# Kernel optimization log

Hardware: AMD Instinct MI355X
Metric: run time of the kernel (lower is better)

The kernel has to match this reference:

```python
import jax, jax.numpy as jnp
import numpy as np

B, S, H, NH, G = 2, 2048, 2048, 16, 2
HD = H // NH          # head_dim = 128
NKV = NH // G         # kv heads = 8
EPS = 1e-6


def setup_inputs() -> dict:
    key = jax.random.key(0)
    ks = jax.random.split(key, 5)
    sc = 0.02
    return {
        "x": jax.random.normal(ks[0], (B, S, H), jnp.float32),
        "wq": jax.random.normal(ks[1], (H, H), jnp.float32) * sc,
        "wk": jax.random.normal(ks[2], (H, H // G), jnp.float32) * sc,
        "wv": jax.random.normal(ks[3], (H, H // G), jnp.float32) * sc,
        "wo": jax.random.normal(ks[4], (H, H), jnp.float32) * sc,
        "rms_w": jnp.ones((HD,), jnp.float32),
        "token_positions": jnp.arange(S, dtype=jnp.int32),
    }


def _rmsnorm(x, w):
    # x: (b, s, HD, n_heads); normalize over the head_dim axis (axis 2)
    ms = jnp.mean(x * x, axis=2, keepdims=True)
    return x * jax.lax.rsqrt(ms + EPS) * w[None, None, :, None]


def _rope(x, pos):
    # x: (b, s, HD, n); interleaved-pair rotation along HD, base 10000
    half = HD // 2
    inv_freq = 1.0 / (10000.0 ** (jnp.arange(half, dtype=jnp.float32) * 2.0 / HD))
    ang = pos.astype(jnp.float32)[:, None] * inv_freq[None, :]   # (s, HD/2)
    cos = jnp.cos(ang)[None, :, :, None]
    sin = jnp.sin(ang)[None, :, :, None]
    x1 = x[:, :, 0::2, :]
    x2 = x[:, :, 1::2, :]
    r1 = x1 * cos - x2 * sin
    r2 = x1 * sin + x2 * cos
    return jnp.stack([r1, r2], axis=3).reshape(x.shape)


def reference(x, wq, wk, wv, wo, rms_w, token_positions):
    b, s, _ = x.shape
    # projections, split hidden as (head_dim, n_heads) exactly like the torch .view
    q = (x @ wq).reshape(b, s, HD, NH)
    k = (x @ wk).reshape(b, s, HD, NKV)
    v = (x @ wv).reshape(b, s, HD, NKV)
    # per-head RMSNorm (over head_dim) then RoPE on Q and K
    q = _rope(_rmsnorm(q, rms_w), token_positions)
    k = _rope(_rmsnorm(k, rms_w), token_positions)
    # grouped-query attention: group G query heads per kv head
    q5 = q.reshape(b, s, HD, NKV, G)
    scores = jnp.einsum('bsdkg,btdk->bkgst', q5, k)          # (b,NKV,G,s,s)
    mask = jnp.triu(jnp.ones((s, s), bool), 1)               # causal
    scores = jnp.where(mask[None, None, None], -jnp.inf, scores)
    attn = jax.nn.softmax(scores / jnp.sqrt(jnp.float32(HD)), axis=-1)
    ctx = jnp.einsum('bkgst,btdk->bkgsd', attn, v)           # (b,NKV,G,s,HD)
    ctx = ctx.reshape(b, NH, s, HD).transpose(0, 2, 1, 3).reshape(b, s, H)
    return ctx @ wo
```

## Files before the change

kernel.cpp:

```cpp
#include <hip/hip_runtime.h>
#include <hip/hip_bf16.h>
#include <stdint.h>

typedef unsigned short u16;
typedef uint32_t u32;
typedef __attribute__((ext_vector_type(8))) short s8v;
typedef __attribute__((ext_vector_type(4))) float f4v;
typedef __attribute__((ext_vector_type(4))) unsigned int u4v;

#define SQ   2048
#define HDIM 2048
#define HD_  128
#define NH_  16
#define NKV_ 8

__device__ __forceinline__ u16 f2b(float f) {
  uint32_t u = __builtin_bit_cast(uint32_t, f);
  u += 0x7fffu + ((u >> 16) & 1u);
  return (u16)(u >> 16);
}
__device__ __forceinline__ float b2f(u16 v) {
  uint32_t u = ((uint32_t)v) << 16;
  return __builtin_bit_cast(float, u);
}
__device__ __forceinline__ u32 pk2(float lo, float hi) {
  return (u32)f2b(lo) | ((u32)f2b(hi) << 16);
}
__device__ __forceinline__ u32 cvtpk(float lo, float hi) {
  u32 r;
  asm("v_cvt_pk_bf16_f32 %0, %1, %2" : "=v"(r) : "v"(lo), "v"(hi));
  return r;
}

__global__ __launch_bounds__(256) void k_cast(const float* __restrict__ in,
                                              u16* __restrict__ out, int n4) {
  int i = blockIdx.x * 256 + threadIdx.x;
  if (i >= n4) return;
  f4v v = *(const f4v*)(in + (size_t)i * 4);
  union { u16 s[4]; uint64_t u; } o;
  o.s[0] = f2b(v[0]); o.s[1] = f2b(v[1]); o.s[2] = f2b(v[2]); o.s[3] = f2b(v[3]);
  *(uint64_t*)(out + (size_t)i * 4) = o.u;
}

__global__ __launch_bounds__(256) void k_transpose4(const float* __restrict__ wq,
                                                    const float* __restrict__ wk,
                                                    const float* __restrict__ wv,
                                                    const float* __restrict__ wo,
                                                    u16* __restrict__ wqt,
                                                    u16* __restrict__ wkt,
                                                    u16* __restrict__ wvt,
                                                    u16* __restrict__ wot) {
  const int z = blockIdx.z;
  const float* in = (z == 0) ? wq : (z == 1) ? wk : (z == 2) ? wv : wo;
  u16* out = (z == 0) ? wqt : (z == 1) ? wkt : (z == 2) ? wvt : wot;
  const int cols = (z == 1 || z == 2) ? 1024 : 2048;
  int c0 = blockIdx.x * 32, r0 = blockIdx.y * 32;
  if (c0 >= cols) return;
  __shared__ float tile[32][33];
  int tx = threadIdx.x & 31, ty = threadIdx.x >> 5;
#pragma unroll
  for (int i = 0; i < 32; i += 8)
    tile[ty + i][tx] = in[(size_t)(r0 + ty + i) * cols + c0 + tx];
  __syncthreads();
#pragma unroll
  for (int i = 0; i < 32; i += 8)
    out[(size_t)(c0 + ty + i) * 2048 + r0 + tx] = f2b(tile[tx][ty + i]);
}

template <int F32OUT>
__global__ __launch_bounds__(256) void k_gemm(const u16* __restrict__ A,
                                              const u16* __restrict__ Bt,
                                              void* __restrict__ C,
                                              int M, int N, int K) {
  __shared__ __align__(16) u16 As[128 * 64];
  __shared__ __align__(16) u16 Bs[128 * 64];
  const int tid = threadIdx.x;
  const int lane = tid & 63, wvi = tid >> 6;
  const int wm = wvi >> 1, wn = wvi & 1;
  const int l15 = lane & 15, l4 = lane >> 4;
  const int m0 = blockIdx.y * 128, n0 = blockIdx.x * 128;
  auto* As3 = (__attribute__((address_space(3))) char*)As;
  auto* Bs3 = (__attribute__((address_space(3))) char*)Bs;
  int srow[4], soff[4];
#pragma unroll
  for (int i = 0; i < 4; i++) {
    int slot = wvi * 4096 + i * 1024 + lane * 16;
    int r = slot >> 7;
    int gc = ((slot >> 4) & 7) ^ (r & 7);
    srow[i] = r; soff[i] = gc * 16;
  }
  f4v acc[4][4] = {};
  for (int k0 = 0; k0 < K; k0 += 64) {
#pragma unroll
    for (int i = 0; i < 4; i++) {
      const char* gA = (const char*)(A + (size_t)(m0 + srow[i]) * K + k0) + soff[i];
      const char* gB = (const char*)(Bt + (size_t)(n0 + srow[i]) * K + k0) + soff[i];
      __builtin_amdgcn_global_load_lds((__attribute__((address_space(1))) void*)gA,
                                       (__attribute__((address_space(3))) void*)(As3 + wvi * 4096 + i * 1024),
                                       16, 0, 0);
      __builtin_amdgcn_global_load_lds((__attribute__((address_space(1))) void*)gB,
                                       (__attribute__((address_space(3))) void*)(Bs3 + wvi * 4096 + i * 1024),
                                       16, 0, 0);
    }
    __syncthreads();
#pragma unroll
    for (int kk = 0; kk < 2; kk++) {
      s8v af[4], bf[4];
#pragma unroll
      for (int i = 0; i < 4; i++) {
        int ra = wm * 64 + i * 16 + l15;
        af[i] = *(const s8v*)((const char*)As + ra * 128 +
                              ((kk * 64 + l4 * 16) ^ ((ra & 7) << 4)));
        int rb = wn * 64 + i * 16 + l15;
        bf[i] = *(const s8v*)((const char*)Bs + rb * 128 +
                              ((kk * 64 + l4 * 16) ^ ((rb & 7) << 4)));
      }
#pragma unroll
      for (int i = 0; i < 4; i++)
#pragma unroll
        for (int j = 0; j < 4; j++)
          acc[i][j] = __builtin_amdgcn_mfma_f32_16x16x32_bf16(af[i], bf[j], acc[i][j], 0, 0, 0);
    }
    __syncthreads();
  }
#pragma unroll
  for (int i = 0; i < 4; i++) {
#pragma unroll
    for (int j = 0; j < 4; j++) {
      int mb = m0 + wm * 64 + i * 16 + l4 * 4;
      int nn = n0 + wn * 64 + j * 16 + l15;
#pragma unroll
      for (int r = 0; r < 4; r++) {
        float v = acc[i][j][r];
        if (F32OUT) ((float*)C)[(size_t)(mb + r) * N + nn] = v;
        else        ((u16*)C)[(size_t)(mb + r) * N + nn]  = f2b(v);
      }
    }
  }
}

__global__ __launch_bounds__(512, 2) void k_gemm256(const u16* __restrict__ A,
                                                    const u16* __restrict__ Bt,
                                                    u16* __restrict__ C,
                                                    int M, int N, int K) {
  __shared__ __align__(16) u16 Al[2][256 * 64];
  __shared__ __align__(16) u16 Bl[2][256 * 64];
  const int tid = threadIdx.x;
  const int lane = tid & 63, wid = tid >> 6;
  const int wm = wid >> 2, wn = wid & 3;
  const int l15 = lane & 15, l4 = lane >> 4;
  const int m0 = blockIdx.y * 256, n0 = blockIdx.x * 256;
  auto* A3 = (__attribute__((address_space(3))) char*)&Al[0][0];
  auto* B3 = (__attribute__((address_space(3))) char*)&Bl[0][0];
  int srow[4], soff[4];
#pragma unroll
  for (int j = 0; j < 4; j++) {
    int slot = j * 8192 + tid * 16;
    srow[j] = slot >> 7;
    soff[j] = (((slot >> 4) & 7) ^ (srow[j] & 7)) * 16;
  }
  int xk2[2];
#pragma unroll
  for (int ks = 0; ks < 2; ks++) xk2[ks] = (((ks * 4 + l4) ^ (l15 & 7)) << 4);

#define STAGE256(buf, k0s)                                                        \
  do {                                                                            \
    _Pragma("unroll")                                                             \
    for (int j = 0; j < 4; j++) {                                                 \
      const char* gA = (const char*)(A + (size_t)(m0 + srow[j]) * K + (k0s)) + soff[j]; \
      __builtin_amdgcn_global_load_lds(                                           \
          (const __attribute__((address_space(1))) void*)gA,                      \
          (__attribute__((address_space(3))) void*)(A3 + (buf) * 32768 + j * 8192 + tid * 16), \
          16, 0, 0);                                                              \
      const char* gB = (const char*)(Bt + (size_t)(n0 + srow[j]) * K + (k0s)) + soff[j]; \
      __builtin_amdgcn_global_load_lds(                                           \
          (const __attribute__((address_space(1))) void*)gB,                      \
          (__attribute__((address_space(3))) void*)(B3 + (buf) * 32768 + j * 8192 + tid * 16), \
          16, 0, 0);                                                              \
    }                                                                             \
  } while (0)

  f4v acc[8][4] = {};
  STAGE256(0, 0);
  STAGE256(1, 64);
  const int nK = K >> 6;
  for (int t = 0; t < nK; t++) {
    if (t == nK - 1) asm volatile("s_waitcnt vmcnt(0)" ::: "memory");
    else             asm volatile("s_waitcnt vmcnt(8)" ::: "memory");
    __builtin_amdgcn_s_barrier();
    __builtin_amdgcn_sched_barrier(0);
    const char* Ab = (const char*)&Al[0][0] + (t & 1) * 32768;
    const char* Bb = (const char*)&Bl[0][0] + (t & 1) * 32768;
#pragma unroll
    for (int qm = 0; qm < 2; qm++)
#pragma unroll
      for (int qn = 0; qn < 2; qn++) {
        s8v af[4][2], bf2[2][2];
#pragma unroll
        for (int i2 = 0; i2 < 4; i2++) {
          int row = wm * 128 + (qm * 4 + i2) * 16 + l15;
#pragma unroll
          for (int ks = 0; ks < 2; ks++)
            af[i2][ks] = *(const s8v*)(Ab + row * 128 + xk2[ks]);
        }
#pragma unroll
        for (int j2 = 0; j2 < 2; j2++) {
          int row = wn * 64 + (qn * 2 + j2) * 16 + l15;
#pragma unroll
          for (int ks = 0; ks < 2; ks++)
            bf2[j2][ks] = *(const s8v*)(Bb + row * 128 + xk2[ks]);
        }
        __builtin_amdgcn_s_setprio(1);
#pragma unroll
        for (int i2 = 0; i2 < 4; i2++)
#pragma unroll
          for (int j2 = 0; j2 < 2; j2++)
#pragma unroll
            for (int ks = 0; ks < 2; ks++)
              acc[qm * 4 + i2][qn * 2 + j2] = __builtin_amdgcn_mfma_f32_16x16x32_bf16(
                  af[i2][ks], bf2[j2][ks], acc[qm * 4 + i2][qn * 2 + j2], 0, 0, 0);
        __builtin_amdgcn_s_setprio(0);
      }
    __builtin_amdgcn_sched_barrier(0);
    if (t + 2 < nK) {
      __builtin_amdgcn_s_barrier();
      STAGE256(t & 1, (t + 2) * 64);
    }
  }
#undef STAGE256
#pragma unroll
  for (int mi = 0; mi < 8; mi++)
#pragma unroll
    for (int ni = 0; ni < 4; ni++) {
      int mb = m0 + wm * 128 + mi * 16 + l4 * 4;
      int nn = n0 + wn * 64 + ni * 16 + l15;
#pragma unroll
      for (int r = 0; r < 4; r++)
        C[(size_t)(mb + r) * N + nn] = f2b(acc[mi][ni][r]);
    }
}

__global__ __launch_bounds__(256) void k_normrope(const u16* __restrict__ qkv,
                                                  const float* __restrict__ rms_w,
                                                  const int* __restrict__ pos_arr,
                                                  u16* __restrict__ qq,
                                                  u16* __restrict__ kko,
                                                  u16* __restrict__ vto) {
  int idx = blockIdx.x;
  int b = idx >> 11, s = idx & 2047;
  int t = threadIdx.x;
  __shared__ float part[256];
  __shared__ float rstdq[16], rstdk[8];
  __shared__ float lcos[64], lsin[64];
  float pos = (float)pos_arr[s];
  if (t < 64) {
    float ang = pos * exp2f(-0.20762050593046f * (float)t);
    float sn, cs;
    sincosf(ang, &sn, &cs);
    lcos[t] = cs; lsin[t] = sn;
  }
  const u16* qr = qkv + (size_t)idx * 4096;
  const u16* kr = qr + 2048;
  const u16* vr = qr + 3072;
  int h = t & 15, ch = t >> 4;
  float qv[8]; float ss = 0.f;
#pragma unroll
  for (int j = 0; j < 8; j++) {
    float v = b2f(qr[(ch * 8 + j) * 16 + h]);
    qv[j] = v; ss += v * v;
  }
  part[t] = ss;
  __syncthreads();
  if (t < 16) {
    float tot = 0.f;
#pragma unroll
    for (int c = 0; c < 16; c++) tot += part[c * 16 + t];
    rstdq[t] = rsqrtf(tot * (1.f / 128.f) + 1e-6f);
  }
  __syncthreads();
  {
    float rs = rstdq[h];
    s8v ov;
#pragma unroll
    for (int p = 0; p < 4; p++) {
      int d0 = ch * 8 + p * 2;
      float v0 = qv[p * 2]     * rs * rms_w[d0];
      float v1 = qv[p * 2 + 1] * rs * rms_w[d0 + 1];
      float cs = lcos[d0 >> 1], sn = lsin[d0 >> 1];
      ov[p * 2]     = (short)f2b((v0 * cs - v1 * sn) * 0.08838834764831845f);
      ov[p * 2 + 1] = (short)f2b((v0 * sn + v1 * cs) * 0.08838834764831845f);
    }
    *(s8v*)(qq + ((size_t)(b * 16 + h) * SQ + s) * HD_ + ch * 8) = ov;
  }
  __syncthreads();
  int kv = t & 7, ch2 = t >> 3;
  float kvs[8]; float ssk = 0.f;
  if (t < 128) {
#pragma unroll
    for (int j = 0; j < 8; j++) {
      float v = b2f(kr[(ch2 * 8 + j) * 8 + kv]);
      kvs[j] = v; ssk += v * v;
    }
    part[t] = ssk;
  }
  __syncthreads();
  if (t < 8) {
    float tot = 0.f;
#pragma unroll
    for (int c = 0; c < 16; c++) tot += part[c * 8 + t];
    rstdk[t] = rsqrtf(tot * (1.f / 128.f) + 1e-6f);
  }
  __syncthreads();
  if (t < 128) {
    float rs = rstdk[kv];
    s8v ov;
#pragma unroll
    for (int p = 0; p < 4; p++) {
      int d0 = ch2 * 8 + p * 2;
      float v0 = kvs[p * 2]     * rs * rms_w[d0];
      float v1 = kvs[p * 2 + 1] * rs * rms_w[d0 + 1];
      float cs = lcos[d0 >> 1], sn = lsin[d0 >> 1];
      ov[p * 2]     = (short)f2b(v0 * cs - v1 * sn);
      ov[p * 2 + 1] = (short)f2b(v0 * sn + v1 * cs);
    }
    *(s8v*)(kko + ((size_t)(b * 8 + kv) * SQ + s) * HD_ + ch2 * 8) = ov;
#pragma unroll
    for (int j = 0; j < 8; j++) {
      int d = ch2 * 8 + j;
      vto[((size_t)(b * 8 + kv) * HD_ + d) * SQ + s] = vr[d * 8 + kv];
    }
  }
}

__global__ __launch_bounds__(512, 2) void k_attn(const u16* __restrict__ qq,
                                                 const u16* __restrict__ kk,
                                                 const u16* __restrict__ vt,
                                                 u16* __restrict__ ctx) {
  const int tile = (blockIdx.z == 1) ? (15 - (int)blockIdx.x) : (int)blockIdx.x;
  const int s0 = tile * 128;
  const int h  = blockIdx.y;
  const int b  = blockIdx.z;
  const int kvh = h >> 1;
  const int tid = threadIdx.x, lane = tid & 63, w = tid >> 6;
  const int l15 = lane & 15, l4 = lane >> 4;
  __shared__ __align__(16) u16 Kl[2][64 * 128];
  __shared__ __align__(16) u16 Vl[2][128 * 64];
  auto* K3 = (__attribute__((address_space(3))) char*)&Kl[0][0];
  auto* V3 = (__attribute__((address_space(3))) char*)&Vl[0][0];
  const u16* qbase = qq + (size_t)(b * 16 + h) * SQ * HD_;
  const u16* kbase = kk + (size_t)(b * 8 + kvh) * SQ * HD_;
  const u16* vbase = vt + (size_t)(b * 8 + kvh) * HD_ * SQ;
  const int swp = s0 + w * 16;
  const int mybound = swp + 16;
  const int ntiles = 2 * tile + 2;

  int krow[2], kgo[2], vrow[2], vgo[2];
#pragma unroll
  for (int j = 0; j < 2; j++) {
    int s = j * 8192 + tid * 16;
    krow[j] = s >> 8;
    kgo[j]  = (((s >> 4) & 15) ^ (krow[j] & 7)) * 8;
    vrow[j] = s >> 7;
    vgo[j]  = (((s >> 4) & 7) ^ (vrow[j] & 7)) * 8;
  }

#define STAGE(buf, t0s)                                                           \
  do {                                                                            \
    _Pragma("unroll")                                                             \
    for (int j = 0; j < 2; j++) {                                                 \
      const u16* gk = kbase + (size_t)((t0s) + krow[j]) * HD_ + kgo[j];           \
      __builtin_amdgcn_global_load_lds(                                           \
          (const __attribute__((address_space(1))) void*)gk,                      \
          (__attribute__((address_space(3))) void*)(K3 + (buf) * 16384 + j * 8192 + tid * 16), \
          16, 0, 0);                                                              \
      const u16* gv = vbase + (size_t)vrow[j] * SQ + (t0s) + vgo[j];              \
      __builtin_amdgcn_global_load_lds(                                           \
          (const __attribute__((address_space(1))) void*)gv,                      \
          (__attribute__((address_space(3))) void*)(V3 + (buf) * 16384 + j * 8192 + tid * 16), \
          16, 0, 0);                                                              \
    }                                                                             \
  } while (0)

  s8v qf[4];
#pragma unroll
  for (int c = 0; c < 4; c++)
    qf[c] = *(const s8v*)(qbase + (size_t)(swp + l15) * HD_ + c * 32 + l4 * 8);

  f4v o[8] = {};
  float m2 = -1e30f, l2 = 0.f;

  const int src1 = ((l4 & 1) << 5) + l15;
  const int src2 = src1 + 16;
  const bool selhi = (l4 >> 1) != 0;
  const int swzk = (l15 & 7);

  int xk[4], xv[2];
#pragma unroll
  for (int c = 0; c < 4; c++) xk[c] = ((c * 4 + l4) ^ swzk) * 8;
#pragma unroll
  for (int ks = 0; ks < 2; ks++) xv[ks] = ((ks * 4 + l4) ^ swzk) * 8;

  STAGE(0, 0);
  STAGE(1, 64);
  int cur = 0;
  for (int i = 0; i < ntiles; i++) {
    const int t0 = i * 64;
    asm volatile("s_waitcnt vmcnt(4)" ::: "memory");
    __builtin_amdgcn_s_barrier();
    __builtin_amdgcn_sched_barrier(0);
    if (t0 < mybound) {
      const u16* kb = &Kl[cur][0];
      const u16* vb = &Vl[cur][0];
      f4v sc[4] = {};
      __builtin_amdgcn_s_setprio(1);
#pragma unroll
      for (int tt = 0; tt < 4; tt++) {
        s8v kf0 = *(const s8v*)(kb + (tt * 16 + l15) * 128 + xk[0]);
        s8v kf1 = *(const s8v*)(kb + (tt * 16 + l15) * 128 + xk[1]);
        s8v kf2 = *(const s8v*)(kb + (tt * 16 + l15) * 128 + xk[2]);
        s8v kf3 = *(const s8v*)(kb + (tt * 16 + l15) * 128 + xk[3]);
        sc[tt] = __builtin_amdgcn_mfma_f32_16x16x32_bf16(kf0, qf[0], sc[tt], 0, 0, 0);
        sc[tt] = __builtin_amdgcn_mfma_f32_16x16x32_bf16(kf1, qf[1], sc[tt], 0, 0, 0);
        sc[tt] = __builtin_amdgcn_mfma_f32_16x16x32_bf16(kf2, qf[2], sc[tt], 0, 0, 0);
        sc[tt] = __builtin_amdgcn_mfma_f32_16x16x32_bf16(kf3, qf[3], sc[tt], 0, 0, 0);
      }
      __builtin_amdgcn_s_setprio(0);
      if (t0 + 63 > swp) {
#pragma unroll
        for (int tt = 0; tt < 4; tt++)
#pragma unroll
          for (int r = 0; r < 4; r++) {
            int tg = t0 + tt * 16 + l4 * 4 + r;
            if (tg > swp + l15) sc[tt][r] = -1e30f;
          }
      }
      float mx = sc[0][0];
#pragma unroll
      for (int tt = 0; tt < 4; tt++)
#pragma unroll
        for (int r = 0; r < 4; r++) mx = fmaxf(mx, sc[tt][r]);
      mx = fmaxf(mx, __shfl_xor(mx, 16));
      mx = fmaxf(mx, __shfl_xor(mx, 32));
      if (__any(mx > m2 + 8.f)) {
        float mn = fmaxf(m2, mx);
        float sf = exp2f((m2 - mn) * 1.44269504f);
        m2 = mn; l2 *= sf;
#pragma unroll
        for (int dd = 0; dd < 8; dd++)
#pragma unroll
          for (int r = 0; r < 4; r++) o[dd][r] *= sf;
      }
      u32 pk[4][2];
      float sum = 0.f;
#pragma unroll
      for (int tt = 0; tt < 4; tt++) {
        float p0 = exp2f((sc[tt][0] - m2) * 1.44269504f);
        float p1 = exp2f((sc[tt][1] - m2) * 1.44269504f);
        float p2 = exp2f((sc[tt][2] - m2) * 1.44269504f);
        float p3 = exp2f((sc[tt][3] - m2) * 1.44269504f);
        sum += (p0 + p1) + (p2 + p3);
        pk[tt][0] = cvtpk(p0, p1);
        pk[tt][1] = cvtpk(p2, p3);
      }
      sum += __shfl_xor(sum, 16);
      sum += __shfl_xor(sum, 32);
      l2 += sum;
      s8v pf[2];
#pragma unroll
      for (int ks = 0; ks < 2; ks++) {
        u32 e00 = (u32)__shfl((int)pk[2 * ks][0], src1);
        u32 e01 = (u32)__shfl((int)pk[2 * ks][1], src1);
        u32 e10 = (u32)__shfl((int)pk[2 * ks + 1][0], src1);
        u32 e11 = (u32)__shfl((int)pk[2 * ks + 1][1], src1);
        u32 f00 = (u32)__shfl((int)pk[2 * ks][0], src2);
        u32 f01 = (u32)__shfl((int)pk[2 * ks][1], src2);
        u32 f10 = (u32)__shfl((int)pk[2 * ks + 1][0], src2);
        u32 f11 = (u32)__shfl((int)pk[2 * ks + 1][1], src2);
        u4v fr;
        fr[0] = selhi ? e10 : e00;
        fr[1] = selhi ? e11 : e01;
        fr[2] = selhi ? f10 : f00;
        fr[3] = selhi ? f11 : f01;
        pf[ks] = __builtin_bit_cast(s8v, fr);
      }
      __builtin_amdgcn_s_setprio(1);
#pragma unroll
      for (int dd = 0; dd < 8; dd++) {
        s8v vf0 = *(const s8v*)(vb + (dd * 16 + l15) * 64 + xv[0]);
        s8v vf1 = *(const s8v*)(vb + (dd * 16 + l15) * 64 + xv[1]);
        o[dd] = __builtin_amdgcn_mfma_f32_16x16x32_bf16(vf0, pf[0], o[dd], 0, 0, 0);
        o[dd] = __builtin_amdgcn_mfma_f32_16x16x32_bf16(vf1, pf[1], o[dd], 0, 0, 0);
      }
      __builtin_amdgcn_s_setprio(0);
    }
    __builtin_amdgcn_sched_barrier(0);
    __builtin_amdgcn_s_barrier();
    if (i + 2 < ntiles) STAGE(cur, t0 + 128);
    cur ^= 1;
  }
#undef STAGE
  float inv = 1.f / l2;
  size_t rowoff = ((size_t)(b * SQ + swp + l15)) * HDIM + h * HD_;
#pragma unroll
  for (int dd = 0; dd < 8; dd++) {
    *(u32*)(ctx + rowoff + dd * 16 + l4 * 4)     = cvtpk(o[dd][0] * inv, o[dd][1] * inv);
    *(u32*)(ctx + rowoff + dd * 16 + l4 * 4 + 2) = cvtpk(o[dd][2] * inv, o[dd][3] * inv);
  }
}

extern "C" void kernel_launch(void* const* d_in, const int* in_sizes, int n_in,
                              void* d_out, int out_size, void* d_ws, size_t ws_size,
                              hipStream_t stream) {
  const float* x     = (const float*)d_in[0];
  const float* wq    = (const float*)d_in[1];
  const float* wk    = (const float*)d_in[2];
  const float* wv    = (const float*)d_in[3];
  const float* wo    = (const float*)d_in[4];
  const float* rms_w = (const float*)d_in[5];
  const int*   pos   = (const int*)d_in[6];

  u16* w = (u16*)d_ws;
  u16* xb   = w;
  u16* wqt  = xb   + 8388608;
  u16* wkt  = wqt  + 4194304;
  u16* wvt  = wkt  + 2097152;
  u16* wot  = wvt  + 2097152;
  u16* qkvraw = wot + 4194304;
  u16* kkb  = qkvraw + 16777216;
  u16* vtb  = kkb  + 4194304;
  u16* qqb  = wqt;
  u16* ctxb = xb;

  k_cast<<<8192, 256, 0, stream>>>(x, xb, 2097152);
  k_transpose4<<<dim3(64, 64, 4), 256, 0, stream>>>(wq, wk, wv, wo, wqt, wkt, wvt, wot);

  k_gemm256<<<dim3(16, 16), 512, 0, stream>>>(xb, wqt, qkvraw, 4096, 4096, 2048);

  k_normrope<<<4096, 256, 0, stream>>>(qkvraw, rms_w, pos, qqb, kkb, vtb);

  k_attn<<<dim3(16, 16, 2), 512, 0, stream>>>(qqb, kkb, vtb, ctxb);

  k_gemm<1><<<dim3(16, 32), 256, 0, stream>>>(ctxb, wot, d_out, 4096, 2048, 2048);
}
```

Measured before the change: 250.5 us.

## Template pipelined 256-row GEMM for output projection and fuse prep kernels

Generalizes the double-buffered 256-row GEMM over the B tile width and output type, and uses a 256x128 variant for the final fp32 output projection instead of the simpler single-buffered 128x128 GEMM. Merges the x cast and weight transposes into one launch to save a kernel launch. Moves the LDS-reuse barriers inside the inner qn loop with an explicit lgkmcnt wait. The added barriers may cost some overlap in the QKV GEMM.

```diff
diff --git a/kernel.cpp b/kernel.cpp
--- a/kernel.cpp
+++ b/kernel.cpp
@@ -23,34 +23,34 @@
   uint32_t u = ((uint32_t)v) << 16;
   return __builtin_bit_cast(float, u);
 }
-__device__ __forceinline__ u32 pk2(float lo, float hi) {
-  return (u32)f2b(lo) | ((u32)f2b(hi) << 16);
-}
 __device__ __forceinline__ u32 cvtpk(float lo, float hi) {
   u32 r;
   asm("v_cvt_pk_bf16_f32 %0, %1, %2" : "=v"(r) : "v"(lo), "v"(hi));
   return r;
 }
 
-__global__ __launch_bounds__(256) void k_cast(const float* __restrict__ in,
-                                              u16* __restrict__ out, int n4) {
-  int i = blockIdx.x * 256 + threadIdx.x;
-  if (i >= n4) return;
-  f4v v = *(const f4v*)(in + (size_t)i * 4);
-  union { u16 s[4]; uint64_t u; } o;
-  o.s[0] = f2b(v[0]); o.s[1] = f2b(v[1]); o.s[2] = f2b(v[2]); o.s[3] = f2b(v[3]);
-  *(uint64_t*)(out + (size_t)i * 4) = o.u;
-}
-
-__global__ __launch_bounds__(256) void k_transpose4(const float* __restrict__ wq,
-                                                    const float* __restrict__ wk,
-                                                    const float* __restrict__ wv,
-                                                    const float* __restrict__ wo,
-                                                    u16* __restrict__ wqt,
-                                                    u16* __restrict__ wkt,
-                                                    u16* __restrict__ wvt,
-                                                    u16* __restrict__ wot) {
+__global__ __launch_bounds__(256) void k_prep(const float* __restrict__ x,
+                                              const float* __restrict__ wq,
+                                              const float* __restrict__ wk,
+                                              const float* __restrict__ wv,
+                                              const float* __restrict__ wo,
+                                              u16* __restrict__ xb,
+                                              u16* __restrict__ wqt,
+                                              u16* __restrict__ wkt,
+                                              u16* __restrict__ wvt,
+                                              u16* __restrict__ wot) {
   const int z = blockIdx.z;
+  if (z == 4) {
+    size_t i = ((size_t)(blockIdx.y * 64 + blockIdx.x) * 256 + threadIdx.x) * 2;
+#pragma unroll
+    for (int j = 0; j < 2; j++) {
+      f4v v = *(const f4v*)(x + (i + j) * 4);
+      union { u16 s[4]; uint64_t u; } o;
+      o.s[0] = f2b(v[0]); o.s[1] = f2b(v[1]); o.s[2] = f2b(v[2]); o.s[3] = f2b(v[3]);
+      *(uint64_t*)(xb + (i + j) * 4) = o.u;
+    }
+    return;
+  }
   const float* in = (z == 0) ? wq : (z == 1) ? wk : (z == 2) ? wv : wo;
   u16* out = (z == 0) ? wqt : (z == 1) ? wkt : (z == 2) ? wvt : wot;
   const int cols = (z == 1 || z == 2) ? 1024 : 2048;
@@ -67,89 +67,21 @@
     out[(size_t)(c0 + ty + i) * 2048 + r0 + tx] = f2b(tile[tx][ty + i]);
 }
 
-template <int F32OUT>
-__global__ __launch_bounds__(256) void k_gemm(const u16* __restrict__ A,
-                                              const u16* __restrict__ Bt,
-                                              void* __restrict__ C,
-                                              int M, int N, int K) {
-  __shared__ __align__(16) u16 As[128 * 64];
-  __shared__ __align__(16) u16 Bs[128 * 64];
-  const int tid = threadIdx.x;
-  const int lane = tid & 63, wvi = tid >> 6;
-  const int wm = wvi >> 1, wn = wvi & 1;
-  const int l15 = lane & 15, l4 = lane >> 4;
-  const int m0 = blockIdx.y * 128, n0 = blockIdx.x * 128;
-  auto* As3 = (__attribute__((address_space(3))) char*)As;
-  auto* Bs3 = (__attribute__((address_space(3))) char*)Bs;
-  int srow[4], soff[4];
-#pragma unroll
-  for (int i = 0; i < 4; i++) {
-    int slot = wvi * 4096 + i * 1024 + lane * 16;
-    int r = slot >> 7;
-    int gc = ((slot >> 4) & 7) ^ (r & 7);
-    srow[i] = r; soff[i] = gc * 16;
-  }
-  f4v acc[4][4] = {};
-  for (int k0 = 0; k0 < K; k0 += 64) {
-#pragma unroll
-    for (int i = 0; i < 4; i++) {
-      const char* gA = (const char*)(A + (size_t)(m0 + srow[i]) * K + k0) + soff[i];
-      const char* gB = (const char*)(Bt + (size_t)(n0 + srow[i]) * K + k0) + soff[i];
-      __builtin_amdgcn_global_load_lds((__attribute__((address_space(1))) void*)gA,
-                                       (__attribute__((address_space(3))) void*)(As3 + wvi * 4096 + i * 1024),
-                                       16, 0, 0);
-      __builtin_amdgcn_global_load_lds((__attribute__((address_space(1))) void*)gB,
-                                       (__attribute__((address_space(3))) void*)(Bs3 + wvi * 4096 + i * 1024),
-                                       16, 0, 0);
-    }
-    __syncthreads();
-#pragma unroll
-    for (int kk = 0; kk < 2; kk++) {
-      s8v af[4], bf[4];
-#pragma unroll
-      for (int i = 0; i < 4; i++) {
-        int ra = wm * 64 + i * 16 + l15;
-        af[i] = *(const s8v*)((const char*)As + ra * 128 +
-                              ((kk * 64 + l4 * 16) ^ ((ra & 7) << 4)));
-        int rb = wn * 64 + i * 16 + l15;
-        bf[i] = *(const s8v*)((const char*)Bs + rb * 128 +
-                              ((kk * 64 + l4 * 16) ^ ((rb & 7) << 4)));
-      }
-#pragma unroll
-      for (int i = 0; i < 4; i++)
-#pragma unroll
-        for (int j = 0; j < 4; j++)
-          acc[i][j] = __builtin_amdgcn_mfma_f32_16x16x32_bf16(af[i], bf[j], acc[i][j], 0, 0, 0);
-    }
-    __syncthreads();
-  }
-#pragma unroll
-  for (int i = 0; i < 4; i++) {
-#pragma unroll
-    for (int j = 0; j < 4; j++) {
-      int mb = m0 + wm * 64 + i * 16 + l4 * 4;
-      int nn = n0 + wn * 64 + j * 16 + l15;
-#pragma unroll
-      for (int r = 0; r < 4; r++) {
-        float v = acc[i][j][r];
-        if (F32OUT) ((float*)C)[(size_t)(mb + r) * N + nn] = v;
-        else        ((u16*)C)[(size_t)(mb + r) * N + nn]  = f2b(v);
-      }
-    }
-  }
-}
-
+template <int BN, int F32OUT>
 __global__ __launch_bounds__(512, 2) void k_gemm256(const u16* __restrict__ A,
                                                     const u16* __restrict__ Bt,
-                                                    u16* __restrict__ C,
+                                                    void* __restrict__ C,
                                                     int M, int N, int K) {
+  constexpr int NB = BN / 64;
+  constexpr int NF = BN / 64;
+  constexpr int NFH = NF / 2;
   __shared__ __align__(16) u16 Al[2][256 * 64];
-  __shared__ __align__(16) u16 Bl[2][256 * 64];
+  __shared__ __align__(16) u16 Bl[2][BN * 64];
   const int tid = threadIdx.x;
   const int lane = tid & 63, wid = tid >> 6;
   const int wm = wid >> 2, wn = wid & 3;
   const int l15 = lane & 15, l4 = lane >> 4;
-  const int m0 = blockIdx.y * 256, n0 = blockIdx.x * 256;
+  const int m0 = blockIdx.y * 256, n0 = blockIdx.x * BN;
   auto* A3 = (__attribute__((address_space(3))) char*)&Al[0][0];
   auto* B3 = (__attribute__((address_space(3))) char*)&Bl[0][0];
   int srow[4], soff[4];
@@ -163,7 +95,7 @@
 #pragma unroll
   for (int ks = 0; ks < 2; ks++) xk2[ks] = (((ks * 4 + l4) ^ (l15 & 7)) << 4);
 
-#define STAGE256(buf, k0s)                                                        \
+#define STAGEAB(buf, k0s)                                                         \
   do {                                                                            \
     _Pragma("unroll")                                                             \
     for (int j = 0; j < 4; j++) {                                                 \
@@ -172,30 +104,34 @@
           (const __attribute__((address_space(1))) void*)gA,                      \
           (__attribute__((address_space(3))) void*)(A3 + (buf) * 32768 + j * 8192 + tid * 16), \
           16, 0, 0);                                                              \
+    }                                                                             \
+    _Pragma("unroll")                                                             \
+    for (int j = 0; j < NB; j++) {                                                \
       const char* gB = (const char*)(Bt + (size_t)(n0 + srow[j]) * K + (k0s)) + soff[j]; \
       __builtin_amdgcn_global_load_lds(                                           \
           (const __attribute__((address_space(1))) void*)gB,                      \
-          (__attribute__((address_space(3))) void*)(B3 + (buf) * 32768 + j * 8192 + tid * 16), \
+          (__attribute__((address_space(3))) void*)(B3 + (buf) * (BN * 128) + j * 8192 + tid * 16), \
           16, 0, 0);                                                              \
     }                                                                             \
   } while (0)
 
-  f4v acc[8][4] = {};
-  STAGE256(0, 0);
-  STAGE256(1, 64);
+  f4v acc[8][NF] = {};
+  STAGEAB(0, 0);
+  STAGEAB(1, 64);
   const int nK = K >> 6;
   for (int t = 0; t < nK; t++) {
     if (t == nK - 1) asm volatile("s_waitcnt vmcnt(0)" ::: "memory");
-    else             asm volatile("s_waitcnt vmcnt(8)" ::: "memory");
+    else if (NB == 4) asm volatile("s_waitcnt vmcnt(8)" ::: "memory");
+    else              asm volatile("s_waitcnt vmcnt(6)" ::: "memory");
     __builtin_amdgcn_s_barrier();
     __builtin_amdgcn_sched_barrier(0);
     const char* Ab = (const char*)&Al[0][0] + (t & 1) * 32768;
-    const char* Bb = (const char*)&Bl[0][0] + (t & 1) * 32768;
+    const char* Bb = (const char*)&Bl[0][0] + (t & 1) * (BN * 128);
 #pragma unroll
     for (int qm = 0; qm < 2; qm++)
 #pragma unroll
       for (int qn = 0; qn < 2; qn++) {
-        s8v af[4][2], bf2[2][2];
+        s8v af[4][2], bf2[NFH][2];
 #pragma unroll
         for (int i2 = 0; i2 < 4; i2++) {
           int row = wm * 128 + (qm * 4 + i2) * 16 + l15;
@@ -204,39 +140,43 @@
             af[i2][ks] = *(const s8v*)(Ab + row * 128 + xk2[ks]);
         }
 #pragma unroll
-        for (int j2 = 0; j2 < 2; j2++) {
-          int row = wn * 64 + (qn * 2 + j2) * 16 + l15;
+        for (int j2 = 0; j2 < NFH; j2++) {
+          int row = wn * (NF * 16) + (qn * NFH + j2) * 16 + l15;
 #pragma unroll
           for (int ks = 0; ks < 2; ks++)
             bf2[j2][ks] = *(const s8v*)(Bb + row * 128 + xk2[ks]);
         }
+        __builtin_amdgcn_s_barrier();
+        asm volatile("s_waitcnt lgkmcnt(0)" ::: "memory");
+        __builtin_amdgcn_sched_barrier(0);
         __builtin_amdgcn_s_setprio(1);
 #pragma unroll
         for (int i2 = 0; i2 < 4; i2++)
 #pragma unroll
-          for (int j2 = 0; j2 < 2; j2++)
+          for (int j2 = 0; j2 < NFH; j2++)
 #pragma unroll
             for (int ks = 0; ks < 2; ks++)
-              acc[qm * 4 + i2][qn * 2 + j2] = __builtin_amdgcn_mfma_f32_16x16x32_bf16(
-                  af[i2][ks], bf2[j2][ks], acc[qm * 4 + i2][qn * 2 + j2], 0, 0, 0);
+              acc[qm * 4 + i2][qn * NFH + j2] = __builtin_amdgcn_mfma_f32_16x16x32_bf16(
+                  af[i2][ks], bf2[j2][ks], acc[qm * 4 + i2][qn * NFH + j2], 0, 0, 0);
         __builtin_amdgcn_s_setprio(0);
-      }
-    __builtin_amdgcn_sched_barrier(0);
-    if (t + 2 < nK) {
-      __builtin_amdgcn_s_barrier();
-      STAGE256(t & 1, (t + 2) * 64);
-    }
-  }
-#undef STAGE256
+        __builtin_amdgcn_sched_barrier(0);
+        __builtin_amdgcn_s_barrier();
+      }
+    if (t + 2 < nK) STAGEAB(t & 1, (t + 2) * 64);
+  }
+#undef STAGEAB
 #pragma unroll
   for (int mi = 0; mi < 8; mi++)
 #pragma unroll
-    for (int ni = 0; ni < 4; ni++) {
+    for (int ni = 0; ni < NF; ni++) {
       int mb = m0 + wm * 128 + mi * 16 + l4 * 4;
-      int nn = n0 + wn * 64 + ni * 16 + l15;
-#pragma unroll
-      for (int r = 0; r < 4; r++)
-        C[(size_t)(mb + r) * N + nn] = f2b(acc[mi][ni][r]);
+      int nn = n0 + wn * (NF * 16) + ni * 16 + l15;
+#pragma unroll
+      for (int r = 0; r < 4; r++) {
+        float v = acc[mi][ni][r];
+        if (F32OUT) ((float*)C)[(size_t)(mb + r) * N + nn] = v;
+        else        ((u16*)C)[(size_t)(mb + r) * N + nn]  = f2b(v);
+      }
     }
 }
 
@@ -531,14 +471,13 @@
   u16* qqb  = wqt;
   u16* ctxb = xb;
 
-  k_cast<<<8192, 256, 0, stream>>>(x, xb, 2097152);
-  k_transpose4<<<dim3(64, 64, 4), 256, 0, stream>>>(wq, wk, wv, wo, wqt, wkt, wvt, wot);
-
-  k_gemm256<<<dim3(16, 16), 512, 0, stream>>>(xb, wqt, qkvraw, 4096, 4096, 2048);
+  k_prep<<<dim3(64, 64, 5), 256, 0, stream>>>(x, wq, wk, wv, wo, xb, wqt, wkt, wvt, wot);
+
+  k_gemm256<256, 0><<<dim3(16, 16), 512, 0, stream>>>(xb, wqt, qkvraw, 4096, 4096, 2048);
 
   k_normrope<<<4096, 256, 0, stream>>>(qkvraw, rms_w, pos, qqb, kkb, vtb);
 
   k_attn<<<dim3(16, 16, 2), 512, 0, stream>>>(qqb, kkb, vtb, ctxb);
 
-  k_gemm<1><<<dim3(16, 32), 256, 0, stream>>>(ctxb, wot, d_out, 4096, 2048, 2048);
-}
+  k_gemm256<128, 1><<<dim3(16, 16), 512, 0, stream>>>(ctxb, wot, d_out, 4096, 2048, 2048);
+}
```

New measurement: 285.9 us. +14.2%, slower.
